# Kernel tuning notes

Hardware: AMD Instinct MI355X
Metric: run time of the kernel (lower is better)

The kernel has to match this reference:

```python
import jax, jax.numpy as jnp
import numpy as np

D_K = 766  # feature dim, also softmax temperature per module init
NEG = -1000000000.0


def setup_inputs() -> dict:
    key = jax.random.key(0)
    k1, k2, k3 = jax.random.split(key, 3)
    B, H, L, D = 2, 4, 2048, D_K
    Q = jax.random.normal(k1, (B, H, L, D), dtype=jnp.float32)
    K = jax.random.normal(k2, (B, H, L, D), dtype=jnp.float32)
    attn_mask = jax.random.randint(k3, (B, H, L, L), 0, 2) > 0  # bool [B,H,Lk,Lq]
    return {"Q": Q, "K": K, "attn_mask": attn_mask}


def reference(Q, K, attn_mask):
    # scores: [B,H,Lq,Lk]
    scores = jnp.einsum("bhqd,bhkd->bhqk", Q, K) / np.sqrt(D_K).astype(np.float32)
    # mask is [B,H,Lk,Lq]; torch applies mask.transpose(2,3)
    scores = jnp.where(jnp.swapaxes(attn_mask, 2, 3), NEG, scores)
    attn1 = jax.nn.softmax(scores, axis=-1)                       # row softmax
    attn2 = jax.nn.softmax(jnp.swapaxes(scores, -1, -2), axis=-1)  # col softmax
    # dropout prob = 0.0 -> identity
    context1 = jnp.einsum("bhqk,bhkd->bhqd", attn1, K)
    context2 = jnp.einsum("bhkq,bhqd->bhkd", attn2, Q)
    return (context1, context2, attn1, attn2)
```

## Files before the change

### kernel.cpp

```cpp
#include <hip/hip_runtime.h>
#include <math.h>

#define L 2048
#define DK 766
#define DKP 768
#define NBH 8
#define NR (NBH * L)
#define NEGV -1000000000.0f

typedef __attribute__((ext_vector_type(8))) short bf16x8_t;
typedef __attribute__((ext_vector_type(4))) float f32x4_t;

#define LDT 72

typedef __attribute__((address_space(1))) const unsigned int gu32;
typedef __attribute__((address_space(3))) unsigned int lu32;

__device__ __forceinline__ short f2bf(float x) {
    union { float f; unsigned u; } v;
    v.f = x;
    unsigned r = v.u + 0x7fff + ((v.u >> 16) & 1);
    return (short)(r >> 16);
}

__device__ __forceinline__ void gl_lds16(const void* g, void* l) {
    __builtin_amdgcn_global_load_lds((gu32*)g, (lu32*)l, 16, 0, 0);
}

#define BARR() asm volatile("s_barrier" ::: "memory")
#define VMW() asm volatile("s_waitcnt vmcnt(0)" ::: "memory")
#define PRIO1() __builtin_amdgcn_s_setprio(1)
#define PRIO0() __builtin_amdgcn_s_setprio(0)

__global__ __launch_bounds__(256) void k_cvtT(const float* __restrict__ Q,
                                              const float* __restrict__ K,
                                              short* __restrict__ Qb,
                                              short* __restrict__ Kb,
                                              short* __restrict__ Qt,
                                              short* __restrict__ Kt) {
    __shared__ short T[64 * LDT];
    const int tz = blockIdx.z;
    const int bh = tz & 7;
    const float* X = (tz < 8) ? Q : K;
    short* Xb = (tz < 8) ? Qb : Kb;
    short* Xt = (tz < 8) ? Qt : Kt;
    X += (size_t)bh * L * DK;
    Xb += (size_t)bh * L * DKP;
    Xt += (size_t)bh * DKP * L;
    const int r0 = blockIdx.y * 64, c0 = blockIdx.x * 64;
    const int t = threadIdx.x;
    const int rl = t >> 2, cc = (t & 3) * 16;

    bf16x8_t v0, v1;
#pragma unroll
    for (int p = 0; p < 8; ++p) {
        int c = c0 + cc + 2 * p;
        float2 f = (c < DK) ? *(const float2*)&X[(size_t)(r0 + rl) * DK + c]
                            : make_float2(0.f, 0.f);
        if (p < 4) { v0[2 * p] = f2bf(f.x); v0[2 * p + 1] = f2bf(f.y); }
        else { v1[2 * (p - 4)] = f2bf(f.x); v1[2 * (p - 4) + 1] = f2bf(f.y); }
    }
    *(bf16x8_t*)&Xb[(size_t)(r0 + rl) * DKP + c0 + cc] = v0;
    *(bf16x8_t*)&Xb[(size_t)(r0 + rl) * DKP + c0 + cc + 8] = v1;
    *(bf16x8_t*)&T[rl * LDT + cc] = v0;
    *(bf16x8_t*)&T[rl * LDT + cc + 8] = v1;
    __syncthreads();
    bf16x8_t w0, w1;
#pragma unroll
    for (int p = 0; p < 8; ++p) {
        w0[p] = T[(cc + p) * LDT + rl];
        w1[p] = T[(cc + 8 + p) * LDT + rl];
    }
    *(bf16x8_t*)&Xt[(size_t)(c0 + rl) * L + r0 + cc] = w0;
    *(bf16x8_t*)&Xt[(size_t)(c0 + rl) * L + r0 + cc + 8] = w1;
}

__global__ __launch_bounds__(256) void k_scoresT(const short* __restrict__ Kb,
                                                 const short* __restrict__ Qb,
                                                 const int* __restrict__ mask,
                                                 float* __restrict__ ST,
                                                 float* __restrict__ prowM,
                                                 float* __restrict__ prowS,
                                                 float* __restrict__ pcolM,
                                                 float* __restrict__ pcolS) {
    __shared__ __align__(16) short As[128 * 64];
    __shared__ __align__(16) short Bs[128 * 64];
    int flat = blockIdx.x + (blockIdx.y << 4) + (blockIdx.z << 8);
    int nw = (flat & 7) * 256 + (flat >> 3);
    const int bxp = nw & 15;
    const int byp = (nw >> 4) & 15;
    const int bh = nw >> 8;

    const short* Am = Kb + (size_t)bh * L * DKP;
    const short* Bm = Qb + (size_t)bh * L * DKP;
    const int* Mm = mask + (size_t)bh * L * L;
    float* Sm = ST + (size_t)bh * L * L;
    const int m0 = byp * 128, n0 = bxp * 128;
    const int t = threadIdx.x, lane = t & 63, wid = t >> 6;
    const int wm = (wid >> 1) * 64, wn = (wid & 1) * 64;
    const int lr = lane & 15, lg = lane >> 4;
    const int lrow = lane >> 3, lcol = lane & 7;

    f32x4_t acc[4][4];
#pragma unroll
    for (int i = 0; i < 4; ++i)
#pragma unroll
        for (int j = 0; j < 4; ++j) acc[i][j] = f32x4_t{0.f, 0.f, 0.f, 0.f};

    for (int k0 = 0; k0 < DKP; k0 += 64) {
#pragma unroll
        for (int g = 0; g < 4; ++g) {
            int row = wid * 32 + g * 8 + lrow;
            gl_lds16(&Am[(size_t)(m0 + row) * DKP + k0 + lcol * 8],
                     (char*)As + wid * 4096 + g * 1024);
            gl_lds16(&Bm[(size_t)(n0 + row) * DKP + k0 + lcol * 8],
                     (char*)Bs + wid * 4096 + g * 1024);
        }
        __syncthreads();
#pragma unroll
        for (int ks = 0; ks < 2; ++ks) {
            bf16x8_t av[4], bv[4];
#pragma unroll
            for (int i = 0; i < 4; ++i)
                av[i] = *(bf16x8_t*)&As[(wm + i * 16 + lr) * 64 + ks * 32 + lg * 8];
#pragma unroll
            for (int j = 0; j < 4; ++j)
                bv[j] = *(bf16x8_t*)&Bs[(wn + j * 16 + lr) * 64 + ks * 32 + lg * 8];
#pragma unroll
            for (int i = 0; i < 4; ++i)
#pragma unroll
                for (int j = 0; j < 4; ++j)
                    acc[i][j] = __builtin_amdgcn_mfma_f32_16x16x32_bf16(
                        av[i], bv[j], acc[i][j], 0, 0, 0);
        }
        __syncthreads();
    }

    const float scale = 1.0f / sqrtf((float)DK);
#pragma unroll
    for (int i = 0; i < 4; ++i) {
        int krow = m0 + wm + i * 16 + lg * 4;
#pragma unroll
        for (int j = 0; j < 4; ++j) {
            int qcol = n0 + wn + j * 16 + lr;
#pragma unroll
            for (int r = 0; r < 4; ++r) {
                int mv = Mm[(size_t)(krow + r) * L + qcol];
                float v = mv ? NEGV : acc[i][j][r] * scale;
                acc[i][j][r] = v;
                Sm[(size_t)(krow + r) * L + qcol] = v;
            }
        }
    }

    float* redb = (float*)As;
#pragma unroll
    for (int i = 0; i < 4; ++i) {
#pragma unroll
        for (int r = 0; r < 4; ++r) {
            float rm = fmaxf(fmaxf(acc[i][0][r], acc[i][1][r]),
                             fmaxf(acc[i][2][r], acc[i][3][r]));
#pragma unroll
            for (int m = 1; m < 16; m <<= 1) rm = fmaxf(rm, __shfl_xor(rm, m, 64));
            float rs = 0.f;
#pragma unroll
            for (int j = 0; j < 4; ++j) rs += expf(acc[i][j][r] - rm);
#pragma unroll
            for (int m = 1; m < 16; m <<= 1) rs += __shfl_xor(rs, m, 64);
            if (lr == 0) {
                int row = wm + i * 16 + lg * 4 + r;
                redb[(wid & 1) * 128 + row] = rm;
                redb[256 + (wid & 1) * 128 + row] = rs;
            }
        }
    }
#pragma unroll
    for (int j = 0; j < 4; ++j) {
        float cm = -INFINITY;
#pragma unroll
        for (int i = 0; i < 4; ++i)
#pragma unroll
            for (int r = 0; r < 4; ++r) cm = fmaxf(cm, acc[i][j][r]);
        cm = fmaxf(cm, __shfl_xor(cm, 16, 64));
        cm = fmaxf(cm, __shfl_xor(cm, 32, 64));
        float cs = 0.f;
#pragma unroll
        for (int i = 0; i < 4; ++i)
#pragma unroll
            for (int r = 0; r < 4; ++r) cs += expf(acc[i][j][r] - cm);
        cs += __shfl_xor(cs, 16, 64);
        cs += __shfl_xor(cs, 32, 64);
        if (lg == 0) {
            int col = wn + j * 16 + lr;
            redb[512 + (wid >> 1) * 128 + col] = cm;
            redb[768 + (wid >> 1) * 128 + col] = cs;
        }
    }
    __syncthreads();
    if (t < 128) {
        float mA = redb[t], mB = redb[128 + t];
        float sA = redb[256 + t], sB = redb[256 + 128 + t];
        float mm = fmaxf(mA, mB);
        float ss = sA * expf(mA - mm) + sB * expf(mB - mm);
        size_t o = (size_t)bxp * NR + bh * L + m0 + t;
        prowM[o] = mm;
        prowS[o] = ss;
    } else {
        int c = t - 128;
        float mA = redb[512 + c], mB = redb[512 + 128 + c];
        float sA = redb[768 + c], sB = redb[768 + 128 + c];
        float mm = fmaxf(mA, mB);
        float ss = sA * expf(mA - mm) + sB * expf(mB - mm);
        size_t o = (size_t)byp * NR + bh * L + n0 + c;
        pcolM[o] = mm;
        pcolS[o] = ss;
    }
}

__global__ __launch_bounds__(256) void k_comb16(const float* __restrict__ prowM,
                                                const float* __restrict__ prowS,
                                                const float* __restrict__ pcolM,
                                                const float* __restrict__ pcolS,
                                                float* __restrict__ m1,
                                                float* __restrict__ r1,
                                                float* __restrict__ m2,
                                                float* __restrict__ r2) {
    int idx = blockIdx.x * 256 + threadIdx.x;
    float m = -INFINITY;
#pragma unroll
    for (int c = 0; c < 16; ++c) m = fmaxf(m, prowM[(size_t)c * NR + idx]);
    float s = 0.f;
#pragma unroll
    for (int c = 0; c < 16; ++c)
        s += prowS[(size_t)c * NR + idx] * expf(prowM[(size_t)c * NR + idx] - m);
    m2[idx] = m;
    r2[idx] = 1.0f / s;

    m = -INFINITY;
#pragma unroll
    for (int c = 0; c < 16; ++c) m = fmaxf(m, pcolM[(size_t)c * NR + idx]);
    s = 0.f;
#pragma unroll
    for (int c = 0; c < 16; ++c)
        s += pcolS[(size_t)c * NR + idx] * expf(pcolM[(size_t)c * NR + idx] - m);
    m1[idx] = m;
    r1[idx] = 1.0f / s;
}

__global__ __launch_bounds__(256) void k_apply(const float* __restrict__ S,
                                               const float* __restrict__ mr,
                                               const float* __restrict__ rr,
                                               const float* __restrict__ mc,
                                               const float* __restrict__ rc,
                                               float* __restrict__ OutIn,
                                               float* __restrict__ OutTr,
                                               short* __restrict__ bIn,
                                               short* __restrict__ bTr) {
    __shared__ float T[64][65];
    const int bh = blockIdx.z;
    const int rb0 = blockIdx.x * 64, cb0 = blockIdx.y * 64;
    const float* Sm = S + (size_t)bh * L * L;
    float* Oin = OutIn + (size_t)bh * L * L;
    float* Otr = OutTr + (size_t)bh * L * L;
    const int t = threadIdx.x, tx = t & 15, ty = t >> 4;

    float4 mcv = *(const float4*)&mc[bh * L + cb0 + tx * 4];
    float4 rcv = *(const float4*)&rc[bh * L + cb0 + tx * 4];

#pragma unroll
    for (int i = 0; i < 4; ++i) {
        int r = rb0 + ty * 4 + i;
        float mrv = mr[bh * L + r], rrv = rr[bh * L + r];
        float4 x = *(const float4*)&Sm[(size_t)r * L + cb0 + tx * 4];
        float4 e = make_float4(expf(x.x - mrv) * rrv, expf(x.y - mrv) * rrv,
                               expf(x.z - mrv) * rrv, expf(x.w - mrv) * rrv);
        *(float4*)&Oin[(size_t)r * L + cb0 + tx * 4] = e;
        short4 b = make_short4(f2bf(e.x), f2bf(e.y), f2bf(e.z), f2bf(e.w));
        *(short4*)&bIn[(size_t)bh * L * L + (size_t)r * L + cb0 + tx * 4] = b;
        T[tx * 4 + 0][ty * 4 + i] = expf(x.x - mcv.x) * rcv.x;
        T[tx * 4 + 1][ty * 4 + i] = expf(x.y - mcv.y) * rcv.y;
        T[tx * 4 + 2][ty * 4 + i] = expf(x.z - mcv.z) * rcv.z;
        T[tx * 4 + 3][ty * 4 + i] = expf(x.w - mcv.w) * rcv.w;
    }
    __syncthreads();
#pragma unroll
    for (int i = 0; i < 4; ++i) {
        int c = ty * 4 + i;
        float4 v = make_float4(T[c][tx * 4], T[c][tx * 4 + 1], T[c][tx * 4 + 2],
                               T[c][tx * 4 + 3]);
        *(float4*)&Otr[(size_t)(cb0 + c) * L + rb0 + tx * 4] = v;
        short4 b = make_short4(f2bf(v.x), f2bf(v.y), f2bf(v.z), f2bf(v.w));
        *(short4*)&bTr[(size_t)bh * L * L + (size_t)(cb0 + c) * L + rb0 + tx * 4] = b;
    }
}

__global__ __launch_bounds__(512, 2) void k_ctx8(const short* __restrict__ a1b,
                                                 const short* __restrict__ a2b,
                                                 const short* __restrict__ Kt,
                                                 const short* __restrict__ Qt,
                                                 float* __restrict__ c1,
                                                 float* __restrict__ c2) {
    __shared__ __align__(16) short LB[65536];

    int flat = blockIdx.x;
    int nw = (flat & 7) * 48 + (flat >> 3);
    int inst = nw / 24, rem = nw % 24;
    int myp = rem / 3, nxp = rem % 3;
    int bh = inst & 7;
    const short* Am = ((inst < 8) ? a1b : a2b) + (size_t)bh * L * L;
    const short* Bt = ((inst < 8) ? Kt : Qt) + (size_t)bh * DKP * L;
    float* Cm = ((inst < 8) ? c1 : c2) + (size_t)bh * L * DK;
    const int m0 = myp * 256, n0 = nxp * 256;

    const int t = threadIdx.x, lane = t & 63, wid = t >> 6;
    const int wr = wid >> 2, wc = wid & 3;
    const int lr = lane & 15, lg = lane >> 4;

    const int schunk = (lane & 7) ^ (lane >> 3);
    const short* aSrc = Am + (size_t)(m0 + wid * 8 + (lane >> 3)) * L + schunk * 8;
    const short* bSrc = Bt + (size_t)(n0 + wid * 8 + (lane >> 3)) * L + schunk * 8;
    char* ldsA = (char*)LB;
    char* ldsB = (char*)LB + 65536;

#define STAGEA(cb, k0n)                                                              \
    do {                                                                             \
        gl_lds16(aSrc + (k0n), ldsA + (cb)*32768 + wid * 1024);                      \
        gl_lds16(aSrc + (size_t)64 * L + (k0n), ldsA + (cb)*32768 + 8192 + wid * 1024); \
        gl_lds16(aSrc + (size_t)128 * L + (k0n), ldsA + (cb)*32768 + 16384 + wid * 1024); \
        gl_lds16(aSrc + (size_t)192 * L + (k0n), ldsA + (cb)*32768 + 24576 + wid * 1024); \
    } while (0)
#define STAGEB(cb, k0n)                                                              \
    do {                                                                             \
        gl_lds16(bSrc + (k0n), ldsB + (cb)*32768 + wid * 1024);                      \
        gl_lds16(bSrc + (size_t)64 * L + (k0n), ldsB + (cb)*32768 + 8192 + wid * 1024); \
        gl_lds16(bSrc + (size_t)128 * L + (k0n), ldsB + (cb)*32768 + 16384 + wid * 1024); \
        gl_lds16(bSrc + (size_t)192 * L + (k0n), ldsB + (cb)*32768 + 24576 + wid * 1024); \
    } while (0)

    const int axr = lr & 7;
    const int kc0 = ((0 + lg) ^ axr) * 8;
    const int kc1 = ((4 + lg) ^ axr) * 8;
    const int aRd = wr * 8192 + lr * 64;
    const int bRd = 32768 + (wc >> 1) * 8192 + ((wc & 1) * 64 + lr) * 64;

#define LDA0(c, i) (*(const bf16x8_t*)&LB[(c)*16384 + aRd + (i)*1024 + kc0])
#define LDA1(c, i) (*(const bf16x8_t*)&LB[(c)*16384 + aRd + (i)*1024 + kc1])
#define LDB0(c, j) (*(const bf16x8_t*)&LB[(c)*16384 + bRd + (j)*1024 + kc0])
#define LDB1(c, j) (*(const bf16x8_t*)&LB[(c)*16384 + bRd + (j)*1024 + kc1])

    f32x4_t acc[8][4];
#pragma unroll
    for (int i = 0; i < 8; ++i)
#pragma unroll
        for (int j = 0; j < 4; ++j) acc[i][j] = f32x4_t{0.f, 0.f, 0.f, 0.f};

    bf16x8_t bfr[4][2];

#define PHASE(c, i0, EXTRA)                                                          \
    do {                                                                             \
        bf16x8_t a00 = LDA0(c, i0), a01 = LDA1(c, i0);                               \
        bf16x8_t a10 = LDA0(c, (i0) + 1), a11 = LDA1(c, (i0) + 1);                   \
        EXTRA;                                                                       \
        BARR();                                                                      \
        PRIO1();                                                                     \
        _Pragma("unroll") for (int j = 0; j < 4; ++j) {                              \
            acc[i0][j] = __builtin_amdgcn_mfma_f32_16x16x32_bf16(a00, bfr[j][0],     \
                                                                 acc[i0][j], 0, 0, 0); \
            acc[i0][j] = __builtin_amdgcn_mfma_f32_16x16x32_bf16(a01, bfr[j][1],     \
                                                                 acc[i0][j], 0, 0, 0); \
            acc[(i0) + 1][j] = __builtin_amdgcn_mfma_f32_16x16x32_bf16(              \
                a10, bfr[j][0], acc[(i0) + 1][j], 0, 0, 0);                          \
            acc[(i0) + 1][j] = __builtin_amdgcn_mfma_f32_16x16x32_bf16(              \
                a11, bfr[j][1], acc[(i0) + 1][j], 0, 0, 0);                          \
        }                                                                            \
        PRIO0();                                                                     \
    } while (0)

    const int NT = L / 64;
    STAGEA(0, 0);
    STAGEB(0, 0);
    VMW();
    BARR();

    for (int kt = 0; kt < NT; ++kt) {
        const int c = kt & 1;
        const bool ds = (kt + 1 < NT);
        const int k0n = (kt + 1) * 64;
#pragma unroll
        for (int j = 0; j < 4; ++j) {
            bfr[j][0] = LDB0(c, j);
            bfr[j][1] = LDB1(c, j);
        }
        PHASE(c, 0, if (ds) STAGEA(c ^ 1, k0n));
        BARR();
        PHASE(c, 2, if (ds) STAGEB(c ^ 1, k0n));
        BARR();
        PHASE(c, 4, ((void)0));
        BARR();
        PHASE(c, 6, ((void)0));
        if (ds) VMW();
        BARR();
    }

#pragma unroll
    for (int i = 0; i < 8; ++i) {
        int row = m0 + wr * 128 + i * 16 + lg * 4;
#pragma unroll
        for (int j = 0; j < 4; ++j) {
            int col = n0 + wc * 64 + j * 16 + lr;
            if (col < DK) {
#pragma unroll
                for (int r = 0; r < 4; ++r)
                    Cm[(size_t)(row + r) * DK + col] = acc[i][j][r];
            }
        }
    }
#undef PHASE
#undef STAGEA
#undef STAGEB
#undef LDA0
#undef LDA1
#undef LDB0
#undef LDB1
}

extern "C" void kernel_launch(void* const* d_in, const int* in_sizes, int n_in,
                              void* d_out, int out_size, void* d_ws, size_t ws_size,
                              hipStream_t stream) {
    const float* Q = (const float*)d_in[0];
    const float* K = (const float*)d_in[1];
    const int* mask = (const int*)d_in[2];
    float* out = (float*)d_out;

    const size_t CTX = (size_t)NBH * L * DK;
    const size_t ATT = (size_t)NBH * L * L;
    float* c1 = out;
    float* c2 = out + CTX;
    float* a1 = out + 2 * CTX;
    float* a2 = out + 2 * CTX + ATT;

    float* ws = (float*)d_ws;
    float* m1 = ws;
    float* r1 = ws + NR;
    float* m2 = ws + 2 * (size_t)NR;
    float* r2 = ws + 3 * (size_t)NR;
    const size_t QBE = (size_t)NBH * L * DKP;
    short* Qb = (short*)(ws + 4 * (size_t)NR);
    short* Kb = Qb + QBE;
    short* a1b = Kb + QBE;
    short* a2b = a1b + ATT;
    short* Qt = a2b + ATT;
    short* Kt = Qt + QBE;

    float* prowM = c1;
    float* prowS = c1 + 16 * (size_t)NR;
    float* pcolM = c1 + 32 * (size_t)NR;
    float* pcolS = c1 + 48 * (size_t)NR;

    dim3 blk(256);

    k_cvtT<<<dim3(12, 32, 16), blk, 0, stream>>>(Q, K, Qb, Kb, Qt, Kt);
    k_scoresT<<<dim3(16, 16, NBH), blk, 0, stream>>>(Kb, Qb, mask, a2, prowM, prowS,
                                                     pcolM, pcolS);
    k_comb16<<<dim3(NR / 256), blk, 0, stream>>>(prowM, prowS, pcolM, pcolS, m1, r1,
                                                 m2, r2);
    k_apply<<<dim3(32, 32, NBH), blk, 0, stream>>>(a2, m2, r2, m1, r1, a2, a1, a2b,
                                                   a1b);
    k_ctx8<<<dim3(384), dim3(512), 0, stream>>>(a1b, a2b, Kt, Qt, c1, c2);
}
```

Baseline: 477.9 us.

## Store masked scores as bf16 and retile context GEMM to 192-wide N tiles

The scores kernel now writes the masked, scaled scores as bf16 into the bf16 attention buffer instead of fp32. The apply kernel reads them back as bf16, which halves the traffic of the score intermediate, and still writes its own bf16 output in place over the same location. Separately, the context GEMM's N tile shrinks from 256 to 192 (3 MFMA column groups per wave, smaller LDS B buffer), so the grid grows from 384 to 512 blocks for better CU balance. The trade-off is some accuracy loss, since the softmax exponent is computed from bf16-rounded scores, and more A-tile reloads across N tiles.

```diff
diff --git a/kernel.cpp b/kernel.cpp
--- a/kernel.cpp
+++ b/kernel.cpp
@@ -21,6 +21,12 @@
     v.f = x;
     unsigned r = v.u + 0x7fff + ((v.u >> 16) & 1);
     return (short)(r >> 16);
+}
+
+__device__ __forceinline__ float bf2f(short s) {
+    union { unsigned u; float f; } v;
+    v.u = ((unsigned)(unsigned short)s) << 16;
+    return v.f;
 }
 
 __device__ __forceinline__ void gl_lds16(const void* g, void* l) {
@@ -78,7 +84,7 @@
 __global__ __launch_bounds__(256) void k_scoresT(const short* __restrict__ Kb,
                                                  const short* __restrict__ Qb,
                                                  const int* __restrict__ mask,
-                                                 float* __restrict__ ST,
+                                                 short* __restrict__ Sb,
                                                  float* __restrict__ prowM,
                                                  float* __restrict__ prowS,
                                                  float* __restrict__ pcolM,
@@ -94,7 +100,7 @@
     const short* Am = Kb + (size_t)bh * L * DKP;
     const short* Bm = Qb + (size_t)bh * L * DKP;
     const int* Mm = mask + (size_t)bh * L * L;
-    float* Sm = ST + (size_t)bh * L * L;
+    short* Sm = Sb + (size_t)bh * L * L;
     const int m0 = byp * 128, n0 = bxp * 128;
     const int t = threadIdx.x, lane = t & 63, wid = t >> 6;
     const int wm = (wid >> 1) * 64, wn = (wid & 1) * 64;
@@ -148,7 +154,7 @@
                 int mv = Mm[(size_t)(krow + r) * L + qcol];
                 float v = mv ? NEGV : acc[i][j][r] * scale;
                 acc[i][j][r] = v;
-                Sm[(size_t)(krow + r) * L + qcol] = v;
+                Sm[(size_t)(krow + r) * L + qcol] = f2bf(v);
             }
         }
     }
@@ -247,7 +253,7 @@
     r1[idx] = 1.0f / s;
 }
 
-__global__ __launch_bounds__(256) void k_apply(const float* __restrict__ S,
+__global__ __launch_bounds__(256) void k_apply(const short* __restrict__ Sb,
                                                const float* __restrict__ mr,
                                                const float* __restrict__ rr,
                                                const float* __restrict__ mc,
@@ -259,7 +265,7 @@
     __shared__ float T[64][65];
     const int bh = blockIdx.z;
     const int rb0 = blockIdx.x * 64, cb0 = blockIdx.y * 64;
-    const float* Sm = S + (size_t)bh * L * L;
+    const short* Sm = Sb + (size_t)bh * L * L;
     float* Oin = OutIn + (size_t)bh * L * L;
     float* Otr = OutTr + (size_t)bh * L * L;
     const int t = threadIdx.x, tx = t & 15, ty = t >> 4;
@@ -271,16 +277,17 @@
     for (int i = 0; i < 4; ++i) {
         int r = rb0 + ty * 4 + i;
         float mrv = mr[bh * L + r], rrv = rr[bh * L + r];
-        float4 x = *(const float4*)&Sm[(size_t)r * L + cb0 + tx * 4];
-        float4 e = make_float4(expf(x.x - mrv) * rrv, expf(x.y - mrv) * rrv,
-                               expf(x.z - mrv) * rrv, expf(x.w - mrv) * rrv);
+        short4 sx = *(const short4*)&Sm[(size_t)r * L + cb0 + tx * 4];
+        float x0 = bf2f(sx.x), x1 = bf2f(sx.y), x2 = bf2f(sx.z), x3 = bf2f(sx.w);
+        float4 e = make_float4(expf(x0 - mrv) * rrv, expf(x1 - mrv) * rrv,
+                               expf(x2 - mrv) * rrv, expf(x3 - mrv) * rrv);
         *(float4*)&Oin[(size_t)r * L + cb0 + tx * 4] = e;
         short4 b = make_short4(f2bf(e.x), f2bf(e.y), f2bf(e.z), f2bf(e.w));
         *(short4*)&bIn[(size_t)bh * L * L + (size_t)r * L + cb0 + tx * 4] = b;
-        T[tx * 4 + 0][ty * 4 + i] = expf(x.x - mcv.x) * rcv.x;
-        T[tx * 4 + 1][ty * 4 + i] = expf(x.y - mcv.y) * rcv.y;
-        T[tx * 4 + 2][ty * 4 + i] = expf(x.z - mcv.z) * rcv.z;
-        T[tx * 4 + 3][ty * 4 + i] = expf(x.w - mcv.w) * rcv.w;
+        T[tx * 4 + 0][ty * 4 + i] = expf(x0 - mcv.x) * rcv.x;
+        T[tx * 4 + 1][ty * 4 + i] = expf(x1 - mcv.y) * rcv.y;
+        T[tx * 4 + 2][ty * 4 + i] = expf(x2 - mcv.z) * rcv.z;
+        T[tx * 4 + 3][ty * 4 + i] = expf(x3 - mcv.w) * rcv.w;
     }
     __syncthreads();
 #pragma unroll
@@ -300,17 +307,17 @@
                                                  const short* __restrict__ Qt,
                                                  float* __restrict__ c1,
                                                  float* __restrict__ c2) {
-    __shared__ __align__(16) short LB[65536];
+    __shared__ __align__(16) short LB[57344];
 
     int flat = blockIdx.x;
-    int nw = (flat & 7) * 48 + (flat >> 3);
-    int inst = nw / 24, rem = nw % 24;
-    int myp = rem / 3, nxp = rem % 3;
+    int nw = (flat & 7) * 64 + (flat >> 3);
+    int inst = nw >> 5, rem = nw & 31;
+    int myp = rem >> 2, nxp = rem & 3;
     int bh = inst & 7;
     const short* Am = ((inst < 8) ? a1b : a2b) + (size_t)bh * L * L;
     const short* Bt = ((inst < 8) ? Kt : Qt) + (size_t)bh * DKP * L;
     float* Cm = ((inst < 8) ? c1 : c2) + (size_t)bh * L * DK;
-    const int m0 = myp * 256, n0 = nxp * 256;
+    const int m0 = myp * 256, n0 = nxp * 192;
 
     const int t = threadIdx.x, lane = t & 63, wid = t >> 6;
     const int wr = wid >> 2, wc = wid & 3;
@@ -322,58 +329,57 @@
     char* ldsA = (char*)LB;
     char* ldsB = (char*)LB + 65536;
 
-#define STAGEA(cb, k0n)                                                              \
-    do {                                                                             \
-        gl_lds16(aSrc + (k0n), ldsA + (cb)*32768 + wid * 1024);                      \
+#define STAGEA(cb, k0n)                                                               \
+    do {                                                                              \
+        gl_lds16(aSrc + (k0n), ldsA + (cb)*32768 + wid * 1024);                       \
         gl_lds16(aSrc + (size_t)64 * L + (k0n), ldsA + (cb)*32768 + 8192 + wid * 1024); \
         gl_lds16(aSrc + (size_t)128 * L + (k0n), ldsA + (cb)*32768 + 16384 + wid * 1024); \
         gl_lds16(aSrc + (size_t)192 * L + (k0n), ldsA + (cb)*32768 + 24576 + wid * 1024); \
     } while (0)
-#define STAGEB(cb, k0n)                                                              \
-    do {                                                                             \
-        gl_lds16(bSrc + (k0n), ldsB + (cb)*32768 + wid * 1024);                      \
-        gl_lds16(bSrc + (size_t)64 * L + (k0n), ldsB + (cb)*32768 + 8192 + wid * 1024); \
-        gl_lds16(bSrc + (size_t)128 * L + (k0n), ldsB + (cb)*32768 + 16384 + wid * 1024); \
-        gl_lds16(bSrc + (size_t)192 * L + (k0n), ldsB + (cb)*32768 + 24576 + wid * 1024); \
+#define STAGEB(cb, k0n)                                                               \
+    do {                                                                              \
+        gl_lds16(bSrc + (k0n), ldsB + (cb)*24576 + wid * 1024);                       \
+        gl_lds16(bSrc + (size_t)64 * L + (k0n), ldsB + (cb)*24576 + 8192 + wid * 1024); \
+        gl_lds16(bSrc + (size_t)128 * L + (k0n), ldsB + (cb)*24576 + 16384 + wid * 1024); \
     } while (0)
 
     const int axr = lr & 7;
     const int kc0 = ((0 + lg) ^ axr) * 8;
     const int kc1 = ((4 + lg) ^ axr) * 8;
     const int aRd = wr * 8192 + lr * 64;
-    const int bRd = 32768 + (wc >> 1) * 8192 + ((wc & 1) * 64 + lr) * 64;
+    const int bRd = 32768 + (wc * 48 + lr) * 64;
 
 #define LDA0(c, i) (*(const bf16x8_t*)&LB[(c)*16384 + aRd + (i)*1024 + kc0])
 #define LDA1(c, i) (*(const bf16x8_t*)&LB[(c)*16384 + aRd + (i)*1024 + kc1])
-#define LDB0(c, j) (*(const bf16x8_t*)&LB[(c)*16384 + bRd + (j)*1024 + kc0])
-#define LDB1(c, j) (*(const bf16x8_t*)&LB[(c)*16384 + bRd + (j)*1024 + kc1])
-
-    f32x4_t acc[8][4];
+#define LDB0(c, j) (*(const bf16x8_t*)&LB[bRd + (c)*12288 + (j)*1024 + kc0])
+#define LDB1(c, j) (*(const bf16x8_t*)&LB[bRd + (c)*12288 + (j)*1024 + kc1])
+
+    f32x4_t acc[8][3];
 #pragma unroll
     for (int i = 0; i < 8; ++i)
 #pragma unroll
-        for (int j = 0; j < 4; ++j) acc[i][j] = f32x4_t{0.f, 0.f, 0.f, 0.f};
-
-    bf16x8_t bfr[4][2];
-
-#define PHASE(c, i0, EXTRA)                                                          \
-    do {                                                                             \
-        bf16x8_t a00 = LDA0(c, i0), a01 = LDA1(c, i0);                               \
-        bf16x8_t a10 = LDA0(c, (i0) + 1), a11 = LDA1(c, (i0) + 1);                   \
-        EXTRA;                                                                       \
-        BARR();                                                                      \
-        PRIO1();                                                                     \
-        _Pragma("unroll") for (int j = 0; j < 4; ++j) {                              \
-            acc[i0][j] = __builtin_amdgcn_mfma_f32_16x16x32_bf16(a00, bfr[j][0],     \
+        for (int j = 0; j < 3; ++j) acc[i][j] = f32x4_t{0.f, 0.f, 0.f, 0.f};
+
+    bf16x8_t bfr[3][2];
+
+#define PHASE(c, i0, EXTRA)                                                           \
+    do {                                                                              \
+        bf16x8_t a00 = LDA0(c, i0), a01 = LDA1(c, i0);                                \
+        bf16x8_t a10 = LDA0(c, (i0) + 1), a11 = LDA1(c, (i0) + 1);                    \
+        EXTRA;                                                                        \
+        BARR();                                                                       \
+        PRIO1();                                                                      \
+        _Pragma("unroll") for (int j = 0; j < 3; ++j) {                               \
+            acc[i0][j] = __builtin_amdgcn_mfma_f32_16x16x32_bf16(a00, bfr[j][0],      \
                                                                  acc[i0][j], 0, 0, 0); \
-            acc[i0][j] = __builtin_amdgcn_mfma_f32_16x16x32_bf16(a01, bfr[j][1],     \
+            acc[i0][j] = __builtin_amdgcn_mfma_f32_16x16x32_bf16(a01, bfr[j][1],      \
                                                                  acc[i0][j], 0, 0, 0); \
-            acc[(i0) + 1][j] = __builtin_amdgcn_mfma_f32_16x16x32_bf16(              \
-                a10, bfr[j][0], acc[(i0) + 1][j], 0, 0, 0);                          \
-            acc[(i0) + 1][j] = __builtin_amdgcn_mfma_f32_16x16x32_bf16(              \
-                a11, bfr[j][1], acc[(i0) + 1][j], 0, 0, 0);                          \
-        }                                                                            \
-        PRIO0();                                                                     \
+            acc[(i0) + 1][j] = __builtin_amdgcn_mfma_f32_16x16x32_bf16(               \
+                a10, bfr[j][0], acc[(i0) + 1][j], 0, 0, 0);                           \
+            acc[(i0) + 1][j] = __builtin_amdgcn_mfma_f32_16x16x32_bf16(               \
+                a11, bfr[j][1], acc[(i0) + 1][j], 0, 0, 0);                           \
+        }                                                                             \
+        PRIO0();                                                                      \
     } while (0)
 
     const int NT = L / 64;
@@ -387,7 +393,7 @@
         const bool ds = (kt + 1 < NT);
         const int k0n = (kt + 1) * 64;
 #pragma unroll
-        for (int j = 0; j < 4; ++j) {
+        for (int j = 0; j < 3; ++j) {
             bfr[j][0] = LDB0(c, j);
             bfr[j][1] = LDB1(c, j);
         }
@@ -406,8 +412,8 @@
     for (int i = 0; i < 8; ++i) {
         int row = m0 + wr * 128 + i * 16 + lg * 4;
 #pragma unroll
-        for (int j = 0; j < 4; ++j) {
-            int col = n0 + wc * 64 + j * 16 + lr;
+        for (int j = 0; j < 3; ++j) {
+            int col = n0 + wc * 48 + j * 16 + lr;
             if (col < DK) {
 #pragma unroll
                 for (int r = 0; r < 4; ++r)
@@ -460,11 +466,11 @@
     dim3 blk(256);
 
     k_cvtT<<<dim3(12, 32, 16), blk, 0, stream>>>(Q, K, Qb, Kb, Qt, Kt);
-    k_scoresT<<<dim3(16, 16, NBH), blk, 0, stream>>>(Kb, Qb, mask, a2, prowM, prowS,
+    k_scoresT<<<dim3(16, 16, NBH), blk, 0, stream>>>(Kb, Qb, mask, a2b, prowM, prowS,
                                                      pcolM, pcolS);
     k_comb16<<<dim3(NR / 256), blk, 0, stream>>>(prowM, prowS, pcolM, pcolS, m1, r1,
                                                  m2, r2);
-    k_apply<<<dim3(32, 32, NBH), blk, 0, stream>>>(a2, m2, r2, m1, r1, a2, a1, a2b,
+    k_apply<<<dim3(32, 32, NBH), blk, 0, stream>>>(a2b, m2, r2, m1, r1, a2, a1, a2b,
                                                    a1b);
-    k_ctx8<<<dim3(384), dim3(512), 0, stream>>>(a1b, a2b, Kt, Qt, c1, c2);
-}
+    k_ctx8<<<dim3(512), dim3(512), 0, stream>>>(a1b, a2b, Kt, Qt, c1, c2);
+}
```

Result: faster. 448.1 us (-6.2%).
